# Optimization experiments

Measured on AMD Instinct MI355X. Metric: run time of the kernel, lower is better.

Reference implementation:

```python
import jax, jax.numpy as jnp
import numpy as np

DEPTH = 3  # args.depth (chemprop default)


def setup_inputs() -> dict:
    key = jax.random.key(0)
    ks = jax.random.split(key, 10)
    n_atoms, n_bonds, max_nb, n_mols = 100000, 200000, 6, 4000
    H, AF, BF = 300, 133, 147  # hidden_size, atom_fdim, bond_fdim

    f_atoms = jax.random.normal(ks[0], (n_atoms, AF), jnp.float32)
    f_bonds = jax.random.normal(ks[1], (n_bonds, BF), jnp.float32)
    a2b = jax.random.randint(ks[2], (n_atoms, max_nb), 0, n_bonds)      # incoming bonds per atom
    b2a = jax.random.randint(ks[3], (n_bonds,), 0, n_atoms)             # source atom per bond
    b2revb = jax.random.randint(ks[4], (n_bonds,), 0, n_bonds)          # reverse bond index
    atom_mol = jnp.sort(jax.random.randint(ks[5], (n_atoms,), 0, n_mols))  # contiguous mol segments (a_scope)

    # Learned params (W_i, W_h bias-free per args.bias=False; W_o has bias)
    W_i = jax.random.normal(ks[6], (BF, H), jnp.float32) * (1.0 / np.sqrt(BF))
    W_h = jax.random.normal(ks[7], (H, H), jnp.float32) * (1.0 / np.sqrt(H))
    W_o = jax.random.normal(ks[8], (AF + H, H), jnp.float32) * (1.0 / np.sqrt(AF + H))
    b_o = jax.random.normal(ks[9], (H,), jnp.float32) * 0.01

    return dict(f_atoms=f_atoms, f_bonds=f_bonds, W_i=W_i, W_h=W_h, W_o=W_o, b_o=b_o,
                a2b=a2b, b2a=b2a, b2revb=b2revb, atom_mol=atom_mol, n_mols=n_mols)


def reference(f_atoms, f_bonds, W_i, W_h, W_o, b_o, a2b, b2a, b2revb, atom_mol, n_mols):
    # Bond-message D-MPNN (atom_messages=False), ReLU activation, dropout=0 (eval)
    inp = f_bonds @ W_i                       # [n_bonds, H]
    message = jax.nn.relu(inp)
    for _ in range(DEPTH - 1):
        nei_a_message = message[a2b]          # [n_atoms, max_nb, H] gather
        a_message = nei_a_message.sum(axis=1) # [n_atoms, H]
        message = a_message[b2a] - message[b2revb]  # [n_bonds, H]
        message = jax.nn.relu(inp + message @ W_h)
    # Atom readout
    a_message = message[a2b].sum(axis=1)      # [n_atoms, H]
    a_input = jnp.concatenate([f_atoms, a_message], axis=1)
    atom_hiddens = jax.nn.relu(a_input @ W_o + b_o)  # [n_atoms, H]
    # Per-molecule mean aggregation (a_scope loop -> segment ops)
    sums = jax.ops.segment_sum(atom_hiddens, atom_mol, num_segments=n_mols)
    counts = jax.ops.segment_sum(jnp.ones((atom_hiddens.shape[0],), atom_hiddens.dtype),
                                 atom_mol, num_segments=n_mols)
    return sums / jnp.maximum(counts, 1.0)[:, None]  # empty mols -> zero vector
```

## Files before the change

### kernel.cpp

```cpp
#include <hip/hip_runtime.h>
#include <hip/hip_bf16.h>
#include <stdint.h>


#define H_DIM 300
#define HP 320
#define AF_DIM 133
#define BF_DIM 147
#define MAXNB 6

typedef __hip_bfloat16 bf16;
typedef __attribute__((ext_vector_type(8))) short short8;
typedef __attribute__((ext_vector_type(4))) float f32x4;

__device__ __forceinline__ float b2f_raw(unsigned short u) {
    union { unsigned int i; float f; } v; v.i = ((unsigned int)u) << 16; return v.f;
}
__device__ __forceinline__ unsigned short f2b_raw(float f) {
    union { float f; unsigned int i; } v; v.f = f;
    unsigned int x = v.i;
    x += 0x7fffu + ((x >> 16) & 1u);
    return (unsigned short)(x >> 16);
}

__device__ __forceinline__ void gload16(const void* g, void* l) {
    __builtin_amdgcn_global_load_lds(
        (const __attribute__((address_space(1))) unsigned int*)g,
        (__attribute__((address_space(3))) unsigned int*)l,
        16, 0, 0);
}

__global__ __launch_bounds__(256) void prep_wt(
    const float* __restrict__ s1, int r1,
    const float* __restrict__ s2, int r2,
    unsigned short* __restrict__ Wt, int nkt)
{
    const int Ktot = nkt * 32;
    const int idx = blockIdx.x * 256 + threadIdx.x;
    if (idx >= 320 * Ktot) return;
    const int n = idx % 320;
    const int k = idx / 320;
    float v = 0.f;
    if (n < H_DIM) {
        if (k < 320) { if (k < r1) v = s1[k * H_DIM + n]; }
        else { const int kk = k - 320; if (kk < r2) v = s2[kk * H_DIM + n]; }
    }
    Wt[n * Ktot + k] = f2b_raw(v);
}

__global__ __launch_bounds__(256) void prep_cvt(
    const float* __restrict__ in, int W,
    unsigned short* __restrict__ outb, int ostride, int M)
{
    const int idx = blockIdx.x * 256 + threadIdx.x;
    if (idx >= M * 20) return;
    const int r = idx / 20;
    const int cc = idx - r * 20;
    uint4 o;
    unsigned short* op = (unsigned short*)&o;
#pragma unroll
    for (int j = 0; j < 8; ++j) {
        const int k = cc * 8 + j;
        op[j] = (k < W) ? f2b_raw(in[(long)r * W + k]) : 0;
    }
    *(uint4*)(outb + (long)r * ostride + cc * 8) = o;
}

template <int NKT, int ASTR, bool RELU_A, bool BIAS_RELU>
__global__ __launch_bounds__(256) void mfma_gemm(
    const unsigned short* __restrict__ Ab,
    const unsigned short* __restrict__ Wt,
    const float* __restrict__ bias,
    bf16* __restrict__ out,
    int M)
{
    constexpr int KTOT = NKT * 32;

    __shared__ char As[2][64 * 64];
    __shared__ char Cs[16 * 640];

    const int t    = threadIdx.x;
    const int m0   = blockIdx.x * 64;
    const int wc   = t >> 6;
    const int lane = t & 63;
    const int l16  = lane & 15;
    const int quad = lane >> 4;

    const int am = t >> 2;
    const int c  = t & 3;
    const int gm = min(m0 + am, M - 1);
    const unsigned short* const agp = Ab + (long)gm * ASTR + c * 8;
    char* const lds0 = As[0] + t * 16;
    char* const lds1 = As[1] + t * 16;

    auto load_b = [&](int kt, short8* bfr) {
        const int kbase = kt * 32 + quad * 8;
#pragma unroll
        for (int nt = 0; nt < 5; ++nt) {
            const int nn = wc * 80 + nt * 16 + l16;
            bfr[nt] = *(const short8*)(Wt + (long)nn * KTOT + kbase);
        }
    };

    f32x4 acc[4][5];
#pragma unroll
    for (int i = 0; i < 4; ++i)
#pragma unroll
        for (int j = 0; j < 5; ++j) acc[i][j] = (f32x4){0.f, 0.f, 0.f, 0.f};

    gload16(agp, lds0);
    __syncthreads();

    for (int kt = 0; kt < NKT; ++kt) {
        short8 bfr[5];
        load_b(kt, bfr);
        if (kt + 1 < NKT)
            gload16(agp + (kt + 1) * 32, ((kt + 1) & 1) ? lds1 : lds0);
        short8 afr[4];
#pragma unroll
        for (int mt = 0; mt < 4; ++mt) {
            short8 v = *(const short8*)(As[kt & 1] + (mt * 16 + l16) * 64 + quad * 16);
            if (RELU_A) {
                unsigned short* rp = (unsigned short*)&v;
#pragma unroll
                for (int j = 0; j < 8; ++j)
                    rp[j] = (rp[j] & 0x8000u) ? 0 : rp[j];
            }
            afr[mt] = v;
        }
#pragma unroll
        for (int nt = 0; nt < 5; ++nt)
#pragma unroll
            for (int mt = 0; mt < 4; ++mt)
                acc[mt][nt] = __builtin_amdgcn_mfma_f32_16x16x32_bf16(
                    afr[mt], bfr[nt], acc[mt][nt], 0, 0, 0);
        __syncthreads();
    }

    for (int mt = 0; mt < 4; ++mt) {
        __syncthreads();
#pragma unroll
        for (int nt = 0; nt < 5; ++nt) {
            const int col = wc * 80 + nt * 16 + l16;
            float bv = 0.f;
            if (BIAS_RELU) bv = (col < H_DIM) ? bias[col] : 0.f;
#pragma unroll
            for (int r = 0; r < 4; ++r) {
                float v = acc[mt][nt][r] + bv;
                if (BIAS_RELU) v = fmaxf(v, 0.f);
                ((unsigned short*)Cs)[(quad * 4 + r) * HP + col] = f2b_raw(v);
            }
        }
        __syncthreads();
        const int gr0 = m0 + mt * 16;
#pragma unroll
        for (int i = 0; i < 3; ++i) {
            const int idx = i * 256 + t;
            if (idx < 640) {
                const int row = idx / 40;
                if (gr0 + row < M)
                    *(uint4*)((char*)out + (long)(gr0 + row) * 640 + (idx - row * 40) * 16)
                        = *(const uint4*)(Cs + idx * 16);
            }
        }
    }
}

__global__ __launch_bounds__(256) void gather_sum_kernel(
    const bf16* __restrict__ msg, const int* __restrict__ a2b,
    unsigned short* __restrict__ amsg, int ostride, int n_atoms)
{
    const int idx = blockIdx.x * 256 + threadIdx.x;
    if (idx >= n_atoms * (HP / 8)) return;
    const int a = idx / (HP / 8);
    const int cc = idx - a * (HP / 8);
    float s[8] = {0.f, 0.f, 0.f, 0.f, 0.f, 0.f, 0.f, 0.f};
    const int base = a * MAXNB;
#pragma unroll
    for (int j = 0; j < MAXNB; ++j) {
        const long b = a2b[base + j];
        const uint4 u = *(const uint4*)((const char*)msg + (b * HP + cc * 8) * 2);
        const unsigned short* up = (const unsigned short*)&u;
#pragma unroll
        for (int e = 0; e < 8; ++e) s[e] += b2f_raw(up[e]);
    }
    uint4 r;
    unsigned short* rp = (unsigned short*)&r;
#pragma unroll
    for (int e = 0; e < 8; ++e) rp[e] = f2b_raw(s[e]);
    *(uint4*)(amsg + (long)a * ostride + cc * 8) = r;
}

__global__ __launch_bounds__(256) void combine_kernel(
    const bf16* __restrict__ inp, const bf16* __restrict__ Gh,
    const bf16* __restrict__ Hm, const int* __restrict__ b2a,
    const int* __restrict__ b2revb, bf16* __restrict__ outm, int n_bonds)
{
    const int idx = blockIdx.x * 256 + threadIdx.x;
    if (idx >= n_bonds * (HP / 8)) return;
    const int b = idx / (HP / 8);
    const int cc = idx - b * (HP / 8);
    const long co = (long)cc * 16;
    const long ra = b2a[b];
    const long rb = b2revb[b];
    const uint4 vi = *(const uint4*)((const char*)inp + (long)b * 640 + co);
    const uint4 vg = *(const uint4*)((const char*)Gh + ra * 640 + co);
    const uint4 vh = *(const uint4*)((const char*)Hm + rb * 640 + co);
    const unsigned short* ip = (const unsigned short*)&vi;
    const unsigned short* gp = (const unsigned short*)&vg;
    const unsigned short* hp = (const unsigned short*)&vh;
    uint4 r;
    unsigned short* rp = (unsigned short*)&r;
#pragma unroll
    for (int e = 0; e < 8; ++e) {
        const float v = b2f_raw(ip[e]) + b2f_raw(gp[e]) - b2f_raw(hp[e]);
        rp[e] = f2b_raw(fmaxf(v, 0.f));
    }
    *(uint4*)((char*)outm + (long)b * 640 + co) = r;
}

__global__ __launch_bounds__(256) void seg_mean_kernel(
    const bf16* __restrict__ hidden, const int* __restrict__ atom_mol,
    float* __restrict__ out, int n_atoms)
{
    const int m = blockIdx.x;
    __shared__ int s_lo, s_hi;
    if (threadIdx.x == 0) {
        int lo = 0, hi = n_atoms;
        while (lo < hi) { int mid = (lo + hi) >> 1; if (atom_mol[mid] < m) lo = mid + 1; else hi = mid; }
        s_lo = lo;
        int lo2 = lo; hi = n_atoms;
        while (lo2 < hi) { int mid = (lo2 + hi) >> 1; if (atom_mol[mid] < m + 1) lo2 = mid + 1; else hi = mid; }
        s_hi = lo2;
    }
    __syncthreads();
    const int lo = s_lo, hi = s_hi;
    const float inv = 1.0f / (float)max(hi - lo, 1);
    for (int cpass = 0; cpass < 2; ++cpass) {
        const int c = cpass * 256 + threadIdx.x;
        if (c >= H_DIM) break;
        float s = 0.f;
        for (int a = lo; a < hi; ++a)
            s += b2f_raw(((const unsigned short*)hidden)[(long)a * HP + c]);
        out[(long)m * H_DIM + c] = s * inv;
    }
}

extern "C" void kernel_launch(void* const* d_in, const int* in_sizes, int n_in,
                              void* d_out, int out_size, void* d_ws, size_t ws_size,
                              hipStream_t stream)
{
    const float* f_atoms = (const float*)d_in[0];
    const float* f_bonds = (const float*)d_in[1];
    const float* W_i     = (const float*)d_in[2];
    const float* W_h     = (const float*)d_in[3];
    const float* W_o     = (const float*)d_in[4];
    const float* b_o     = (const float*)d_in[5];
    const int*  a2b      = (const int*)d_in[6];
    const int*  b2a      = (const int*)d_in[7];
    const int*  b2revb   = (const int*)d_in[8];
    const int*  atom_mol = (const int*)d_in[9];

    const int n_atoms = in_sizes[0] / AF_DIM;
    const int n_bonds = in_sizes[1] / BF_DIM;
    const int n_mols  = out_size / H_DIM;

    char* ws = (char*)d_ws;
    size_t off = 0;
    auto alloc = [&](size_t bytes) {
        size_t o = off; off += (bytes + 255) & ~(size_t)255; return o;
    };
    bf16* inpB = (bf16*)(ws + alloc((size_t)n_bonds * HP * 2));
    bf16* msgX = (bf16*)(ws + alloc((size_t)n_bonds * HP * 2));
    bf16* HmB  = (bf16*)(ws + alloc((size_t)n_bonds * HP * 2));
    bf16* amsg = (bf16*)(ws + alloc((size_t)n_atoms * HP * 2));
    unsigned short* Wt1 = (unsigned short*)(ws + alloc(320 * 160 * 2));
    unsigned short* WtH = (unsigned short*)(ws + alloc(320 * 320 * 2));
    unsigned short* Wt3 = (unsigned short*)(ws + alloc(320 * 480 * 2));
    unsigned short* fb16    = (unsigned short*)HmB;
    unsigned short* atomcat = (unsigned short*)inpB;
    bf16* hidden = HmB;

    const dim3 blk(256);

    prep_wt<<<(320 * 160 + 255) / 256, blk, 0, stream>>>(W_i, BF_DIM, nullptr, 0, Wt1, 5);
    prep_wt<<<(320 * 320 + 255) / 256, blk, 0, stream>>>(W_h, H_DIM, nullptr, 0, WtH, 10);
    prep_wt<<<(320 * 480 + 255) / 256, blk, 0, stream>>>(W_o + (size_t)AF_DIM * H_DIM, H_DIM,
                                                         W_o, AF_DIM, Wt3, 15);

    const int gB = (n_bonds + 63) / 64;
    const int gA = (n_atoms + 63) / 64;
    const int gG = (n_atoms * (HP / 8) + 255) / 256;
    const int gC = (n_bonds * (HP / 8) + 255) / 256;

    prep_cvt<<<(n_bonds * 20 + 255) / 256, blk, 0, stream>>>(f_bonds, BF_DIM, fb16, 160, n_bonds);

    mfma_gemm<5, 160, false, false><<<gB, blk, 0, stream>>>(fb16, Wt1, nullptr, inpB, n_bonds);

    mfma_gemm<10, 320, true, false><<<gB, blk, 0, stream>>>(
        (const unsigned short*)inpB, WtH, nullptr, HmB, n_bonds);
    gather_sum_kernel<<<gG, blk, 0, stream>>>(HmB, a2b, (unsigned short*)amsg, HP, n_atoms);
    combine_kernel<<<gC, blk, 0, stream>>>(inpB, amsg, HmB, b2a, b2revb, msgX, n_bonds);

    mfma_gemm<10, 320, false, false><<<gB, blk, 0, stream>>>(
        (const unsigned short*)msgX, WtH, nullptr, HmB, n_bonds);
    gather_sum_kernel<<<gG, blk, 0, stream>>>(HmB, a2b, (unsigned short*)amsg, HP, n_atoms);
    combine_kernel<<<gC, blk, 0, stream>>>(inpB, amsg, HmB, b2a, b2revb, msgX, n_bonds);

    prep_cvt<<<(n_atoms * 20 + 255) / 256, blk, 0, stream>>>(f_atoms, AF_DIM, atomcat + 320, 480, n_atoms);
    gather_sum_kernel<<<gG, blk, 0, stream>>>(msgX, a2b, atomcat, 480, n_atoms);
    mfma_gemm<15, 480, false, true><<<gA, blk, 0, stream>>>(atomcat, Wt3, b_o, hidden, n_atoms);

    seg_mean_kernel<<<n_mols, blk, 0, stream>>>(hidden, atom_mol, (float*)d_out, n_atoms);
}
```

Measured before the change: 1.040 ms.

## Double GEMM K-step per barrier and parallelize segment mean over atom rows

The MFMA GEMM now stages two 32-wide K slices per iteration, which halves the number of __syncthreads barriers and loop iterations. To fit this, the K dimensions of W_i and the atom-concat input are padded to multiples of 64 (192 and 512). The segment-mean kernel now reads rows as 16-byte vectors across 6 row groups and reduces partial sums in LDS, replacing the scalar per-column loop over atoms. The extra padding adds a little more memory traffic and some zero MFMA work.

```diff
diff --git a/kernel.cpp b/kernel.cpp
--- a/kernel.cpp
+++ b/kernel.cpp
@@ -50,12 +50,12 @@
 
 __global__ __launch_bounds__(256) void prep_cvt(
     const float* __restrict__ in, int W,
-    unsigned short* __restrict__ outb, int ostride, int M)
+    unsigned short* __restrict__ outb, int ostride, int CH, int M)
 {
     const int idx = blockIdx.x * 256 + threadIdx.x;
-    if (idx >= M * 20) return;
-    const int r = idx / 20;
-    const int cc = idx - r * 20;
+    if (idx >= M * CH) return;
+    const int r = idx / CH;
+    const int cc = idx - r * CH;
     uint4 o;
     unsigned short* op = (unsigned short*)&o;
 #pragma unroll
@@ -66,7 +66,7 @@
     *(uint4*)(outb + (long)r * ostride + cc * 8) = o;
 }
 
-template <int NKT, int ASTR, bool RELU_A, bool BIAS_RELU>
+template <int NKT2, int ASTR, bool RELU_A, bool BIAS_RELU>
 __global__ __launch_bounds__(256) void mfma_gemm(
     const unsigned short* __restrict__ Ab,
     const unsigned short* __restrict__ Wt,
@@ -74,9 +74,9 @@
     bf16* __restrict__ out,
     int M)
 {
-    constexpr int KTOT = NKT * 32;
-
-    __shared__ char As[2][64 * 64];
+    constexpr int KTOT = NKT2 * 64;
+
+    __shared__ char As[2][2][64 * 64];
     __shared__ char Cs[16 * 640];
 
     const int t    = threadIdx.x;
@@ -90,11 +90,19 @@
     const int c  = t & 3;
     const int gm = min(m0 + am, M - 1);
     const unsigned short* const agp = Ab + (long)gm * ASTR + c * 8;
-    char* const lds0 = As[0] + t * 16;
-    char* const lds1 = As[1] + t * 16;
-
-    auto load_b = [&](int kt, short8* bfr) {
-        const int kbase = kt * 32 + quad * 8;
+    char* const d0s0 = As[0][0] + t * 16;
+    char* const d0s1 = As[0][1] + t * 16;
+    char* const d1s0 = As[1][0] + t * 16;
+    char* const d1s1 = As[1][1] + t * 16;
+
+    auto stage = [&](int kt, int buf) {
+        const unsigned short* g = agp + kt * 64;
+        gload16(g,      buf ? d1s0 : d0s0);
+        gload16(g + 32, buf ? d1s1 : d0s1);
+    };
+
+    auto load_b = [&](int kt, int s, short8* bfr) {
+        const int kbase = kt * 64 + s * 32 + quad * 8;
 #pragma unroll
         for (int nt = 0; nt < 5; ++nt) {
             const int nn = wc * 80 + nt * 16 + l16;
@@ -108,23 +116,22 @@
 #pragma unroll
         for (int j = 0; j < 5; ++j) acc[i][j] = (f32x4){0.f, 0.f, 0.f, 0.f};
 
-    gload16(agp, lds0);
+    stage(0, 0);
     __syncthreads();
 
-    for (int kt = 0; kt < NKT; ++kt) {
-        short8 bfr[5];
-        load_b(kt, bfr);
-        if (kt + 1 < NKT)
-            gload16(agp + (kt + 1) * 32, ((kt + 1) & 1) ? lds1 : lds0);
+    for (int kt = 0; kt < NKT2; ++kt) {
+        const char* const abase = (kt & 1) ? As[1][0] : As[0][0];
+        short8 b0[5];
+        load_b(kt, 0, b0);
+        if (kt + 1 < NKT2) stage(kt + 1, (kt + 1) & 1);
         short8 afr[4];
 #pragma unroll
         for (int mt = 0; mt < 4; ++mt) {
-            short8 v = *(const short8*)(As[kt & 1] + (mt * 16 + l16) * 64 + quad * 16);
+            short8 v = *(const short8*)(abase + (mt * 16 + l16) * 64 + quad * 16);
             if (RELU_A) {
                 unsigned short* rp = (unsigned short*)&v;
 #pragma unroll
-                for (int j = 0; j < 8; ++j)
-                    rp[j] = (rp[j] & 0x8000u) ? 0 : rp[j];
+                for (int j = 0; j < 8; ++j) rp[j] = (rp[j] & 0x8000u) ? 0 : rp[j];
             }
             afr[mt] = v;
         }
@@ -133,7 +140,25 @@
 #pragma unroll
             for (int mt = 0; mt < 4; ++mt)
                 acc[mt][nt] = __builtin_amdgcn_mfma_f32_16x16x32_bf16(
-                    afr[mt], bfr[nt], acc[mt][nt], 0, 0, 0);
+                    afr[mt], b0[nt], acc[mt][nt], 0, 0, 0);
+        short8 b1[5];
+        load_b(kt, 1, b1);
+#pragma unroll
+        for (int mt = 0; mt < 4; ++mt) {
+            short8 v = *(const short8*)(abase + 4096 + (mt * 16 + l16) * 64 + quad * 16);
+            if (RELU_A) {
+                unsigned short* rp = (unsigned short*)&v;
+#pragma unroll
+                for (int j = 0; j < 8; ++j) rp[j] = (rp[j] & 0x8000u) ? 0 : rp[j];
+            }
+            afr[mt] = v;
+        }
+#pragma unroll
+        for (int nt = 0; nt < 5; ++nt)
+#pragma unroll
+            for (int mt = 0; mt < 4; ++mt)
+                acc[mt][nt] = __builtin_amdgcn_mfma_f32_16x16x32_bf16(
+                    afr[mt], b1[nt], acc[mt][nt], 0, 0, 0);
         __syncthreads();
     }
 
@@ -224,8 +249,10 @@
     float* __restrict__ out, int n_atoms)
 {
     const int m = blockIdx.x;
+    const int t = threadIdx.x;
     __shared__ int s_lo, s_hi;
-    if (threadIdx.x == 0) {
+    __shared__ float sb[6][320];
+    if (t == 0) {
         int lo = 0, hi = n_atoms;
         while (lo < hi) { int mid = (lo + hi) >> 1; if (atom_mol[mid] < m) lo = mid + 1; else hi = mid; }
         s_lo = lo;
@@ -235,14 +262,26 @@
     }
     __syncthreads();
     const int lo = s_lo, hi = s_hi;
+    if (t < 240) {
+        const int ra = t / 40;
+        const int c  = t - ra * 40;
+        float s[8] = {0.f, 0.f, 0.f, 0.f, 0.f, 0.f, 0.f, 0.f};
+        for (int a = lo + ra; a < hi; a += 6) {
+            const uint4 u = *(const uint4*)((const char*)hidden + (long)a * 640 + c * 16);
+            const unsigned short* up = (const unsigned short*)&u;
+#pragma unroll
+            for (int e = 0; e < 8; ++e) s[e] += b2f_raw(up[e]);
+        }
+#pragma unroll
+        for (int e = 0; e < 8; ++e) sb[ra][c * 8 + e] = s[e];
+    }
+    __syncthreads();
     const float inv = 1.0f / (float)max(hi - lo, 1);
-    for (int cpass = 0; cpass < 2; ++cpass) {
-        const int c = cpass * 256 + threadIdx.x;
-        if (c >= H_DIM) break;
+    for (int cc = t; cc < H_DIM; cc += 256) {
         float s = 0.f;
-        for (int a = lo; a < hi; ++a)
-            s += b2f_raw(((const unsigned short*)hidden)[(long)a * HP + c]);
-        out[(long)m * H_DIM + c] = s * inv;
+#pragma unroll
+        for (int r = 0; r < 6; ++r) s += sb[r][cc];
+        out[(long)m * H_DIM + cc] = s * inv;
     }
 }
 
@@ -274,42 +313,42 @@
     bf16* msgX = (bf16*)(ws + alloc((size_t)n_bonds * HP * 2));
     bf16* HmB  = (bf16*)(ws + alloc((size_t)n_bonds * HP * 2));
     bf16* amsg = (bf16*)(ws + alloc((size_t)n_atoms * HP * 2));
-    unsigned short* Wt1 = (unsigned short*)(ws + alloc(320 * 160 * 2));
+    unsigned short* Wt1 = (unsigned short*)(ws + alloc(320 * 192 * 2));
     unsigned short* WtH = (unsigned short*)(ws + alloc(320 * 320 * 2));
-    unsigned short* Wt3 = (unsigned short*)(ws + alloc(320 * 480 * 2));
+    unsigned short* Wt3 = (unsigned short*)(ws + alloc(320 * 512 * 2));
     unsigned short* fb16    = (unsigned short*)HmB;
     unsigned short* atomcat = (unsigned short*)inpB;
     bf16* hidden = HmB;
 
     const dim3 blk(256);
 
-    prep_wt<<<(320 * 160 + 255) / 256, blk, 0, stream>>>(W_i, BF_DIM, nullptr, 0, Wt1, 5);
+    prep_wt<<<(320 * 192 + 255) / 256, blk, 0, stream>>>(W_i, BF_DIM, nullptr, 0, Wt1, 6);
     prep_wt<<<(320 * 320 + 255) / 256, blk, 0, stream>>>(W_h, H_DIM, nullptr, 0, WtH, 10);
-    prep_wt<<<(320 * 480 + 255) / 256, blk, 0, stream>>>(W_o + (size_t)AF_DIM * H_DIM, H_DIM,
-                                                         W_o, AF_DIM, Wt3, 15);
+    prep_wt<<<(320 * 512 + 255) / 256, blk, 0, stream>>>(W_o + (size_t)AF_DIM * H_DIM, H_DIM,
+                                                         W_o, AF_DIM, Wt3, 16);
 
     const int gB = (n_bonds + 63) / 64;
     const int gA = (n_atoms + 63) / 64;
     const int gG = (n_atoms * (HP / 8) + 255) / 256;
     const int gC = (n_bonds * (HP / 8) + 255) / 256;
 
-    prep_cvt<<<(n_bonds * 20 + 255) / 256, blk, 0, stream>>>(f_bonds, BF_DIM, fb16, 160, n_bonds);
-
-    mfma_gemm<5, 160, false, false><<<gB, blk, 0, stream>>>(fb16, Wt1, nullptr, inpB, n_bonds);
-
-    mfma_gemm<10, 320, true, false><<<gB, blk, 0, stream>>>(
+    prep_cvt<<<(n_bonds * 24 + 255) / 256, blk, 0, stream>>>(f_bonds, BF_DIM, fb16, 192, 24, n_bonds);
+
+    mfma_gemm<3, 192, false, false><<<gB, blk, 0, stream>>>(fb16, Wt1, nullptr, inpB, n_bonds);
+
+    mfma_gemm<5, 320, true, false><<<gB, blk, 0, stream>>>(
         (const unsigned short*)inpB, WtH, nullptr, HmB, n_bonds);
     gather_sum_kernel<<<gG, blk, 0, stream>>>(HmB, a2b, (unsigned short*)amsg, HP, n_atoms);
     combine_kernel<<<gC, blk, 0, stream>>>(inpB, amsg, HmB, b2a, b2revb, msgX, n_bonds);
 
-    mfma_gemm<10, 320, false, false><<<gB, blk, 0, stream>>>(
+    mfma_gemm<5, 320, false, false><<<gB, blk, 0, stream>>>(
         (const unsigned short*)msgX, WtH, nullptr, HmB, n_bonds);
     gather_sum_kernel<<<gG, blk, 0, stream>>>(HmB, a2b, (unsigned short*)amsg, HP, n_atoms);
     combine_kernel<<<gC, blk, 0, stream>>>(inpB, amsg, HmB, b2a, b2revb, msgX, n_bonds);
 
-    prep_cvt<<<(n_atoms * 20 + 255) / 256, blk, 0, stream>>>(f_atoms, AF_DIM, atomcat + 320, 480, n_atoms);
-    gather_sum_kernel<<<gG, blk, 0, stream>>>(msgX, a2b, atomcat, 480, n_atoms);
-    mfma_gemm<15, 480, false, true><<<gA, blk, 0, stream>>>(atomcat, Wt3, b_o, hidden, n_atoms);
+    prep_cvt<<<(n_atoms * 24 + 255) / 256, blk, 0, stream>>>(f_atoms, AF_DIM, atomcat + 320, 512, 24, n_atoms);
+    gather_sum_kernel<<<gG, blk, 0, stream>>>(msgX, a2b, atomcat, 512, n_atoms);
+    mfma_gemm<8, 512, false, true><<<gA, blk, 0, stream>>>(atomcat, Wt3, b_o, hidden, n_atoms);
 
     seg_mean_kernel<<<n_mols, blk, 0, stream>>>(hidden, atom_mol, (float*)d_out, n_atoms);
 }
```

After: 1.045 ms. About the same (+0.5%).
